# Kernel optimization log

Measured on AMD Instinct MI355X. Metric: run time of the kernel, lower is better.

Reference implementation:

```python
import jax, jax.numpy as jnp
import numpy as np
import math

B, L, D, H = 2, 2048, 1024, 16
HD = D // H          # head_dim = 64
DF = 4096            # d_feedforward
SIGMA = 0.02


def setup_inputs() -> dict:
    key = jax.random.key(0)
    ks = jax.random.split(key, 18)
    g = lambda k, shape: (jax.random.normal(k, shape, jnp.float32) * SIGMA)
    inp = {
        "x": jax.random.normal(ks[0], (B, L, D), jnp.float32),
        # causal mask: True above diagonal -> masked
        "causal_mask": jnp.triu(jnp.ones((L, L), dtype=bool), 1),
        # attention weights, stored [in, out] (math-equivalent to torch Linear)
        "Wq": g(ks[1], (D, D)), "bq": jnp.zeros((D,), jnp.float32),
        "Wk": g(ks[2], (D, D)), "bk": jnp.zeros((D,), jnp.float32),
        "Wv": g(ks[3], (D, D)), "bv": jnp.zeros((D,), jnp.float32),
        "Wo": g(ks[4], (D, D)), "bo": jnp.zeros((D,), jnp.float32),
        "ln1_g": jnp.ones((D,), jnp.float32), "ln1_b": jnp.zeros((D,), jnp.float32),
        "W1": g(ks[5], (D, DF)), "b1": jnp.zeros((DF,), jnp.float32),
        "W2": g(ks[6], (DF, D)), "b2": jnp.zeros((D,), jnp.float32),
        "ln2_g": jnp.ones((D,), jnp.float32), "ln2_b": jnp.zeros((D,), jnp.float32),
    }
    return inp


def _layernorm(x, g, b, eps=1e-5):
    m = jnp.mean(x, axis=-1, keepdims=True)
    v = jnp.mean((x - m) ** 2, axis=-1, keepdims=True)
    return (x - m) * jax.lax.rsqrt(v + eps) * g + b


def _rita_gelu(h):
    return h * 0.5 * (1.0 + jnp.tanh(0.79788456 * h * (1.0 + 0.044715 * h * h)))


def _rotate_half(x):
    x1, x2 = x[..., : x.shape[-1] // 2], x[..., x.shape[-1] // 2 :]
    return jnp.concatenate((-x2, x1), axis=-1)


def _rope_tables(seq_len, head_dim, dtype):
    inv_freq = 1.0 / (10000.0 ** (jnp.arange(0, head_dim, 2, dtype=jnp.float32) / head_dim))
    t = jnp.arange(seq_len, dtype=jnp.float32)
    freqs = jnp.einsum("i,j->ij", t, inv_freq)          # [L, HD/2]
    emb = jnp.concatenate((freqs, freqs), axis=-1)        # [L, HD]
    return jnp.cos(emb).astype(dtype)[None, None], jnp.sin(emb).astype(dtype)[None, None]


def reference(x, causal_mask, Wq, bq, Wk, bk, Wv, bv, Wo, bo,
              ln1_g, ln1_b, W1, b1, W2, b2, ln2_g, ln2_b):
    N, Lx, Dx = x.shape
    # --- attention block ---
    y = _layernorm(x, ln1_g, ln1_b)
    def heads(t):  # [N,L,D] -> [N,H,L,HD]
        return t.reshape(N, Lx, H, HD).transpose(0, 2, 1, 3)
    q = heads(y @ Wq + bq)
    k = heads(y @ Wk + bk)
    v = heads(y @ Wv + bv)
    cos, sin = _rope_tables(Lx, HD, x.dtype)
    q = q * cos + _rotate_half(q) * sin
    k = k * cos + _rotate_half(k) * sin
    att = jnp.einsum("nhqd,nhkd->nhqk", q, k) * (1.0 / math.sqrt(HD))
    att = jnp.where(causal_mask[None, None], jnp.float32(-jnp.inf).astype(att.dtype), att)
    att = jax.nn.softmax(att, axis=-1)
    o = jnp.einsum("nhqk,nhkd->nhqd", att, v)
    o = o.transpose(0, 2, 1, 3).reshape(N, Lx, Dx)
    y = o @ Wo + bo
    x = x + y
    # --- MLP block ---
    y = _layernorm(x, ln2_g, ln2_b)
    y = _rita_gelu(y @ W1 + b1) @ W2 + b2
    return x + y
```

## Files before the change

kernel.cpp:

```cpp
#include <hip/hip_runtime.h>
#include <math.h>

#define B_  2
#define L_  2048
#define D_  1024
#define H_  16
#define HD_ 64
#define DF_ 4096
#define NR_ 4096

typedef __bf16 bf16_t;
typedef bf16_t bf16x8 __attribute__((ext_vector_type(8)));
typedef float  f32x4  __attribute__((ext_vector_type(4)));
typedef unsigned short u16;
typedef u16 u16x8 __attribute__((ext_vector_type(8)));
typedef u16 u16x4 __attribute__((ext_vector_type(4)));

__device__ __forceinline__ u16 f2bf(float f) {
  unsigned u = __float_as_uint(f);
  u += 0x7fffu + ((u >> 16) & 1u);
  return (u16)(u >> 16);
}
__device__ __forceinline__ float bf2f(u16 s) {
  return __uint_as_float(((unsigned)s) << 16);
}
__device__ __forceinline__ float gelu_f(float h) {
  return h * 0.5f * (1.f + tanhf(0.79788456f * h * (1.f + 0.044715f * h * h)));
}

__device__ __forceinline__ void async_copy16(void* lds, const void* g) {
  __builtin_amdgcn_global_load_lds(
      (const __attribute__((address_space(1))) unsigned int*)g,
      (__attribute__((address_space(3))) unsigned int*)lds, 16, 0, 0);
}

__global__ __launch_bounds__(256) void transpose_conv(
    const float* __restrict__ W, u16* __restrict__ out, int K, int N) {
  __shared__ float T[64][65];
  const int tid = threadIdx.x;
  const int n0 = blockIdx.x * 64, k0 = blockIdx.y * 64;
  const int r = tid >> 2, c4 = (tid & 3) * 16;
  const float* src = W + (size_t)(k0 + r) * N + n0 + c4;
#pragma unroll
  for (int i = 0; i < 16; i += 4) {
    float4 f = *(const float4*)(src + i);
    T[r][c4 + i + 0] = f.x; T[r][c4 + i + 1] = f.y;
    T[r][c4 + i + 2] = f.z; T[r][c4 + i + 3] = f.w;
  }
  __syncthreads();
  u16* dst = out + (size_t)(n0 + r) * K + k0 + c4;
#pragma unroll
  for (int half = 0; half < 2; ++half) {
    u16x8 o8;
#pragma unroll
    for (int i = 0; i < 8; ++i) o8[i] = f2bf(T[c4 + half * 8 + i][r]);
    *(u16x8*)(dst + half * 8) = o8;
  }
}

__global__ __launch_bounds__(256) void concat_bias(
    const float* __restrict__ bq, const float* __restrict__ bk,
    const float* __restrict__ bv, float* __restrict__ bqkv) {
  int i = blockIdx.x * 256 + threadIdx.x;
  if (i < 3072) {
    float v = (i < 1024) ? bq[i] : (i < 2048) ? bk[i - 1024] : bv[i - 2048];
    bqkv[i] = v;
  }
}

__global__ __launch_bounds__(256) void rope_tables(
    float* __restrict__ cosT, float* __restrict__ sinT) {
  int i = blockIdx.x * 256 + threadIdx.x;
  int pos = i >> 5, d = i & 31;
  float invf = powf(10000.f, -(float)d / 32.f);
  float a = (float)pos * invf;
  cosT[i] = cosf(a);
  sinT[i] = sinf(a);
}

__global__ __launch_bounds__(256) void rope_apply(
    u16* __restrict__ qkv, const float* __restrict__ cosT,
    const float* __restrict__ sinT) {
  int i = blockIdx.x * 256 + threadIdx.x;
  int d0 = (i & 3) * 8;
  int hh = (i >> 2) & 15;
  int qk = (i >> 6) & 1;
  int row = i >> 7;
  int pos = row & (L_ - 1);
  size_t base = (size_t)row * 3072 + qk * 1024 + hh * 64 + d0;
  u16x8 a = *(const u16x8*)(qkv + base);
  u16x8 bb = *(const u16x8*)(qkv + base + 32);
  float4 c0 = *(const float4*)(cosT + pos * 32 + d0);
  float4 c1 = *(const float4*)(cosT + pos * 32 + d0 + 4);
  float4 s0 = *(const float4*)(sinT + pos * 32 + d0);
  float4 s1 = *(const float4*)(sinT + pos * 32 + d0 + 4);
  const float qs = qk ? 1.f : 0.125f;
  u16x8 ra, rb;
#pragma unroll
  for (int j = 0; j < 8; ++j) {
    float co = (j < 4) ? ((const float*)&c0)[j] : ((const float*)&c1)[j - 4];
    float si = (j < 4) ? ((const float*)&s0)[j] : ((const float*)&s1)[j - 4];
    float v0 = bf2f(a[j]), v1 = bf2f(bb[j]);
    ra[j] = f2bf((v0 * co - v1 * si) * qs);
    rb[j] = f2bf((v1 * co + v0 * si) * qs);
  }
  *(u16x8*)(qkv + base) = ra;
  *(u16x8*)(qkv + base + 32) = rb;
}

__global__ __launch_bounds__(256) void v_transpose(
    const u16* __restrict__ qkv, u16* __restrict__ vt) {
  const int tid = threadIdx.x;
  const int d = tid & 63, sub = tid >> 6;
  const int s0 = (blockIdx.x * 4 + sub) * 8;
  const int bh = blockIdx.y, b = bh >> 4, h = bh & 15;
  u16x8 o;
#pragma unroll
  for (int i = 0; i < 8; ++i)
    o[i] = qkv[(size_t)(b * L_ + s0 + i) * 3072 + 2048 + h * 64 + d];
  *(u16x8*)(vt + ((size_t)bh * 64 + d) * 2048 + s0) = o;
}

__global__ __launch_bounds__(256) void ln_kernel(
    const float* __restrict__ x, const float* __restrict__ gm,
    const float* __restrict__ bt, u16* __restrict__ out) {
  const int row = blockIdx.x, tid = threadIdx.x;
  const float4 v = ((const float4*)(x + (size_t)row * D_))[tid];
  float s = v.x + v.y + v.z + v.w;
#pragma unroll
  for (int m = 1; m < 64; m <<= 1) s += __shfl_xor(s, m);
  __shared__ float red[4], red2[4];
  if ((tid & 63) == 0) red[tid >> 6] = s;
  __syncthreads();
  const float mean = (red[0] + red[1] + red[2] + red[3]) * (1.f / D_);
  float d0 = v.x - mean, d1 = v.y - mean, d2 = v.z - mean, d3 = v.w - mean;
  float sq = d0 * d0 + d1 * d1 + d2 * d2 + d3 * d3;
#pragma unroll
  for (int m = 1; m < 64; m <<= 1) sq += __shfl_xor(sq, m);
  if ((tid & 63) == 0) red2[tid >> 6] = sq;
  __syncthreads();
  const float var = (red2[0] + red2[1] + red2[2] + red2[3]) * (1.f / D_);
  const float rstd = rsqrtf(var + 1e-5f);
  const int c = tid * 4;
  u16x4 o;
  o[0] = f2bf(d0 * rstd * gm[c + 0] + bt[c + 0]);
  o[1] = f2bf(d1 * rstd * gm[c + 1] + bt[c + 1]);
  o[2] = f2bf(d2 * rstd * gm[c + 2] + bt[c + 2]);
  o[3] = f2bf(d3 * rstd * gm[c + 3] + bt[c + 3]);
  ((u16x4*)(out + (size_t)row * D_))[tid] = o;
}

template <int EPI>
__global__ __launch_bounds__(256) void gemm_bt(
    const u16* __restrict__ A, const u16* __restrict__ Bt,
    const float* __restrict__ bias, const float* __restrict__ resid,
    void* __restrict__ out, int M, int N, int K) {
  __shared__ u16 As[128 * 32];
  __shared__ u16 Bs[128 * 32];
  const int tid = threadIdx.x;
  const int l = tid & 63, wid = tid >> 6;
  const int m0 = blockIdx.y * 128, n0 = blockIdx.x * 128;
  const int wr = wid >> 1, wc = wid & 1;

  f32x4 acc[4][4];
#pragma unroll
  for (int mi = 0; mi < 4; ++mi)
#pragma unroll
    for (int ni = 0; ni < 4; ++ni) acc[mi][ni] = (f32x4){0.f, 0.f, 0.f, 0.f};

  for (int kb = 0; kb < K; kb += 32) {
#pragma unroll
    for (int r = 0; r < 2; ++r) {
      const int fo = r * 4096 + tid * 16;
      const int row = fo >> 6, cb = fo & 63;
      async_copy16((char*)As + fo, A + (size_t)(m0 + row) * K + kb + (cb >> 1));
      async_copy16((char*)Bs + fo, Bt + (size_t)(n0 + row) * K + kb + (cb >> 1));
    }
    __syncthreads();
    bf16x8 ag[4], bg[4];
#pragma unroll
    for (int mi = 0; mi < 4; ++mi) {
      int row = wr * 64 + mi * 16 + (l & 15);
      ag[mi] = *(const bf16x8*)((const char*)As + row * 64 + ((l >> 4) * 16));
    }
#pragma unroll
    for (int ni = 0; ni < 4; ++ni) {
      int row = wc * 64 + ni * 16 + (l & 15);
      bg[ni] = *(const bf16x8*)((const char*)Bs + row * 64 + ((l >> 4) * 16));
    }
#pragma unroll
    for (int mi = 0; mi < 4; ++mi)
#pragma unroll
      for (int ni = 0; ni < 4; ++ni)
        acc[mi][ni] = __builtin_amdgcn_mfma_f32_16x16x32_bf16(
            ag[mi], bg[ni], acc[mi][ni], 0, 0, 0);
    __syncthreads();
  }

  const int cl = l & 15, rq = l >> 4;
#pragma unroll
  for (int ni = 0; ni < 4; ++ni) {
    const int col = n0 + wc * 64 + ni * 16 + cl;
    const float bv = bias[col];
#pragma unroll
    for (int mi = 0; mi < 4; ++mi) {
#pragma unroll
      for (int j = 0; j < 4; ++j) {
        const int rowg = m0 + wr * 64 + mi * 16 + rq * 4 + j;
        float v = acc[mi][ni][j] + bv;
        if (EPI == 0) {
          ((u16*)out)[(size_t)rowg * N + col] = f2bf(v);
        } else if (EPI == 1) {
          ((u16*)out)[(size_t)rowg * N + col] = f2bf(gelu_f(v));
        } else {
          ((float*)out)[(size_t)rowg * N + col] =
              v + resid[(size_t)rowg * N + col];
        }
      }
    }
  }
}

__global__ __launch_bounds__(256, 4) void attn_kernel(
    const u16* __restrict__ qkv, const u16* __restrict__ vt,
    u16* __restrict__ o) {
  const int tid = threadIdx.x, l = tid & 63, wid = tid >> 6;
  const int id = blockIdx.x;
  const int seq = id >> 3, xcd = id & 7;
  const int bh = xcd * 4 + (seq & 3);
  const int qblk = 31 - (seq >> 2);
  const int b = bh >> 4, h = bh & 15;
  const int q0 = qblk * 64;
  __shared__ u16 Ps[4][16 * 64];

  const int qrow_g = b * L_ + q0 + wid * 16 + (l & 15);
  const u16* qp = qkv + (size_t)qrow_g * 3072 + h * 64 + ((l >> 4) * 8);
  const bf16x8 qa0 = *(const bf16x8*)qp;
  const bf16x8 qa1 = *(const bf16x8*)(qp + 32);

  const u16* kbase = qkv + (size_t)(b * L_ + (l & 15)) * 3072 + 1024 + h * 64 +
                     ((l >> 4) * 8);
  const u16* vbase = vt + ((size_t)bh * 64 + (l & 15)) * 2048 + ((l >> 4) * 8);

  float m_[4], ls[4];
  f32x4 oa[4];
#pragma unroll
  for (int j = 0; j < 4; ++j) { m_[j] = -1e30f; ls[j] = 0.f; }
#pragma unroll
  for (int t = 0; t < 4; ++t) oa[t] = (f32x4){0.f, 0.f, 0.f, 0.f};

  char* const psw = (char*)&Ps[wid][0];
  const int rq4 = (l >> 4) << 2;

  for (int kb = 0; kb <= q0; kb += 64) {
    const bool diag = (kb == q0);

    bf16x8 kf[4][2];
#pragma unroll
    for (int t = 0; t < 4; ++t) {
      const u16* kp = kbase + (size_t)(kb + t * 16) * 3072;
      kf[t][0] = *(const bf16x8*)kp;
      kf[t][1] = *(const bf16x8*)(kp + 32);
    }

    float p[4][4];
#pragma unroll
    for (int t = 0; t < 4; ++t) {
      f32x4 s = (f32x4){0.f, 0.f, 0.f, 0.f};
      s = __builtin_amdgcn_mfma_f32_16x16x32_bf16(qa0, kf[t][0], s, 0, 0, 0);
      s = __builtin_amdgcn_mfma_f32_16x16x32_bf16(qa1, kf[t][1], s, 0, 0, 0);
      if (diag) {
        const int kcol = t * 16 + (l & 15);
        const int qrow = wid * 16 + rq4;
#pragma unroll
        for (int j = 0; j < 4; ++j)
          p[t][j] = (kcol <= qrow + j) ? s[j] : -1e30f;
      } else {
#pragma unroll
        for (int j = 0; j < 4; ++j) p[t][j] = s[j];
      }
    }

#pragma unroll
    for (int j = 0; j < 4; ++j) {
      float pm = fmaxf(fmaxf(p[0][j], p[1][j]), fmaxf(p[2][j], p[3][j]));
      pm = fmaxf(pm, __shfl_xor(pm, 1));
      pm = fmaxf(pm, __shfl_xor(pm, 2));
      pm = fmaxf(pm, __shfl_xor(pm, 4));
      pm = fmaxf(pm, __shfl_xor(pm, 8));
      const float mn = fmaxf(m_[j], pm);
      const float sc = __expf(m_[j] - mn);
      float rs = 0.f;
#pragma unroll
      for (int t = 0; t < 4; ++t) { p[t][j] = __expf(p[t][j] - mn); rs += p[t][j]; }
      rs += __shfl_xor(rs, 1);
      rs += __shfl_xor(rs, 2);
      rs += __shfl_xor(rs, 4);
      rs += __shfl_xor(rs, 8);
      ls[j] = ls[j] * sc + rs;
      m_[j] = mn;
#pragma unroll
      for (int t = 0; t < 4; ++t) oa[t][j] *= sc;
    }

#pragma unroll
    for (int t = 0; t < 4; ++t)
#pragma unroll
      for (int j = 0; j < 4; ++j) {
        const int rr = rq4 + j, cc = t * 16 + (l & 15);
        *(u16*)(psw + rr * 128 + ((cc * 2) ^ ((rr & 7) << 4))) = f2bf(p[t][j]);
      }

    bf16x8 vf[4][2];
#pragma unroll
    for (int t = 0; t < 4; ++t) {
      const u16* vp = vbase + (size_t)t * 16 * 2048 + kb;
      vf[t][0] = *(const bf16x8*)vp;
      vf[t][1] = *(const bf16x8*)(vp + 32);
    }

#pragma unroll
    for (int kc = 0; kc < 2; ++kc) {
      const int pr = l & 15, ke = kc * 32 + ((l >> 4) * 8);
      bf16x8 pf = *(const bf16x8*)(psw + pr * 128 + ((ke * 2) ^ ((pr & 7) << 4)));
#pragma unroll
      for (int t = 0; t < 4; ++t)
        oa[t] = __builtin_amdgcn_mfma_f32_16x16x32_bf16(pf, vf[t][kc], oa[t], 0, 0, 0);
    }
  }

#pragma unroll
  for (int j = 0; j < 4; ++j) {
    const float inv = 1.f / ls[j];
    const int rowg = b * L_ + q0 + wid * 16 + rq4 + j;
    u16* op = o + (size_t)rowg * D_ + h * 64 + (l & 15);
#pragma unroll
    for (int t = 0; t < 4; ++t) op[t * 16] = f2bf(oa[t][j] * inv);
  }
}

extern "C" void kernel_launch(void* const* d_in, const int* in_sizes, int n_in,
                              void* d_out, int out_size, void* d_ws, size_t ws_size,
                              hipStream_t stream) {
  (void)in_sizes; (void)n_in; (void)out_size; (void)ws_size;
  const float* x    = (const float*)d_in[0];
  const float* Wq   = (const float*)d_in[2];
  const float* bq   = (const float*)d_in[3];
  const float* Wk   = (const float*)d_in[4];
  const float* bk   = (const float*)d_in[5];
  const float* Wv   = (const float*)d_in[6];
  const float* bv   = (const float*)d_in[7];
  const float* Wo   = (const float*)d_in[8];
  const float* bo   = (const float*)d_in[9];
  const float* ln1g = (const float*)d_in[10];
  const float* ln1b = (const float*)d_in[11];
  const float* W1   = (const float*)d_in[12];
  const float* b1   = (const float*)d_in[13];
  const float* W2   = (const float*)d_in[14];
  const float* b2   = (const float*)d_in[15];
  const float* ln2g = (const float*)d_in[16];
  const float* ln2b = (const float*)d_in[17];
  float* out = (float*)d_out;
  char* ws = (char*)d_ws;

  u16*   wqkvT = (u16*)(ws + 0);
  u16*   woT   = (u16*)(ws + 6291456);
  u16*   w1T   = (u16*)(ws + 8388608);
  u16*   w2T   = (u16*)(ws + 16777216);
  float* bqkv  = (float*)(ws + 25165824);
  float* cosT  = (float*)(ws + 25178112);
  float* sinT  = (float*)(ws + 25440256);
  float* x2    = (float*)(ws + 25702400);
  u16*   lnbuf = (u16*)(ws + 42479616);
  u16*   vtb   = lnbuf;
  u16*   qkv   = (u16*)(ws + 50868224);
  u16*   attnO = (u16*)(ws + 76034048);
  u16*   hbuf  = qkv;

  const dim3 blk(256);
  transpose_conv<<<dim3(16, 16), blk, 0, stream>>>(Wq, wqkvT, 1024, 1024);
  transpose_conv<<<dim3(16, 16), blk, 0, stream>>>(Wk, wqkvT + 1024 * 1024, 1024, 1024);
  transpose_conv<<<dim3(16, 16), blk, 0, stream>>>(Wv, wqkvT + 2048 * 1024, 1024, 1024);
  transpose_conv<<<dim3(16, 16), blk, 0, stream>>>(Wo, woT, 1024, 1024);
  transpose_conv<<<dim3(64, 16), blk, 0, stream>>>(W1, w1T, 1024, 4096);
  transpose_conv<<<dim3(16, 64), blk, 0, stream>>>(W2, w2T, 4096, 1024);
  concat_bias<<<12, blk, 0, stream>>>(bq, bk, bv, bqkv);
  rope_tables<<<256, blk, 0, stream>>>(cosT, sinT);

  ln_kernel<<<NR_, blk, 0, stream>>>(x, ln1g, ln1b, lnbuf);
  gemm_bt<0><<<dim3(24, 32), blk, 0, stream>>>(lnbuf, wqkvT, bqkv, nullptr,
                                               qkv, NR_, 3072, 1024);
  rope_apply<<<2048, blk, 0, stream>>>(qkv, cosT, sinT);
  v_transpose<<<dim3(64, 32), blk, 0, stream>>>(qkv, vtb);
  attn_kernel<<<1024, blk, 0, stream>>>(qkv, vtb, attnO);

  gemm_bt<2><<<dim3(8, 32), blk, 0, stream>>>(attnO, woT, bo, x, x2,
                                              NR_, 1024, 1024);
  ln_kernel<<<NR_, blk, 0, stream>>>(x2, ln2g, ln2b, lnbuf);
  gemm_bt<1><<<dim3(32, 32), blk, 0, stream>>>(lnbuf, w1T, b1, nullptr,
                                               hbuf, NR_, 4096, 1024);
  gemm_bt<2><<<dim3(8, 32), blk, 0, stream>>>(hbuf, w2T, b2, x2, out,
                                              NR_, 1024, 4096);
}
```

Before: 549.8 us.

## Split-K atomic GEMMs for N=1024 projections and restructure attention softmax

The two N=1024 GEMMs (Wo and W2) become split-K launches with 2 and 4 K-slices. Their partial results are added with float atomics into an output that a new kernel pre-fills with residual plus bias. This targets low occupancy, since only 256 tiles cover the GPU. Attention is also rewritten to use transposed MFMA operands so each lane owns one query row, with the log2e scale folded into the Q scaling and exp2f used in softmax. This removes most cross-lane shuffles and skips fully masked diagonal tiles. The atomics make the results nondeterministic and add an extra elementwise pass over memory.

```diff
diff --git a/kernel.cpp b/kernel.cpp
--- a/kernel.cpp
+++ b/kernel.cpp
@@ -15,6 +15,8 @@
 typedef unsigned short u16;
 typedef u16 u16x8 __attribute__((ext_vector_type(8)));
 typedef u16 u16x4 __attribute__((ext_vector_type(4)));
+typedef unsigned int u32;
+typedef u32 u32x2 __attribute__((ext_vector_type(2)));
 
 __device__ __forceinline__ u16 f2bf(float f) {
   unsigned u = __float_as_uint(f);
@@ -94,7 +96,7 @@
   float4 c1 = *(const float4*)(cosT + pos * 32 + d0 + 4);
   float4 s0 = *(const float4*)(sinT + pos * 32 + d0);
   float4 s1 = *(const float4*)(sinT + pos * 32 + d0 + 4);
-  const float qs = qk ? 1.f : 0.125f;
+  const float qs = qk ? 1.f : 0.18033688f;
   u16x8 ra, rb;
 #pragma unroll
   for (int j = 0; j < 8; ++j) {
@@ -150,17 +152,30 @@
   ((u16x4*)(out + (size_t)row * D_))[tid] = o;
 }
 
+__global__ __launch_bounds__(256) void bias_resid_init(
+    const float* __restrict__ resid, const float* __restrict__ bias,
+    float* __restrict__ out) {
+  int i = blockIdx.x * 256 + threadIdx.x;
+  int c4 = (i & 255) * 4;
+  float4 r = ((const float4*)resid)[i];
+  float4 bv = *(const float4*)(bias + c4);
+  r.x += bv.x; r.y += bv.y; r.z += bv.z; r.w += bv.w;
+  ((float4*)out)[i] = r;
+}
+
 template <int EPI>
 __global__ __launch_bounds__(256) void gemm_bt(
     const u16* __restrict__ A, const u16* __restrict__ Bt,
-    const float* __restrict__ bias, const float* __restrict__ resid,
-    void* __restrict__ out, int M, int N, int K) {
+    const float* __restrict__ bias, void* __restrict__ out,
+    int M, int N, int K) {
   __shared__ u16 As[128 * 32];
   __shared__ u16 Bs[128 * 32];
   const int tid = threadIdx.x;
   const int l = tid & 63, wid = tid >> 6;
   const int m0 = blockIdx.y * 128, n0 = blockIdx.x * 128;
   const int wr = wid >> 1, wc = wid & 1;
+  const int ksub = K / gridDim.z;
+  const int k0 = blockIdx.z * ksub;
 
   f32x4 acc[4][4];
 #pragma unroll
@@ -168,7 +183,7 @@
 #pragma unroll
     for (int ni = 0; ni < 4; ++ni) acc[mi][ni] = (f32x4){0.f, 0.f, 0.f, 0.f};
 
-  for (int kb = 0; kb < K; kb += 32) {
+  for (int kb = k0; kb < k0 + ksub; kb += 32) {
 #pragma unroll
     for (int r = 0; r < 2; ++r) {
       const int fo = r * 4096 + tid * 16;
@@ -201,7 +216,7 @@
 #pragma unroll
   for (int ni = 0; ni < 4; ++ni) {
     const int col = n0 + wc * 64 + ni * 16 + cl;
-    const float bv = bias[col];
+    const float bv = (EPI == 3) ? 0.f : bias[col];
 #pragma unroll
     for (int mi = 0; mi < 4; ++mi) {
 #pragma unroll
@@ -213,8 +228,7 @@
         } else if (EPI == 1) {
           ((u16*)out)[(size_t)rowg * N + col] = f2bf(gelu_f(v));
         } else {
-          ((float*)out)[(size_t)rowg * N + col] =
-              v + resid[(size_t)rowg * N + col];
+          atomicAdd(&((float*)out)[(size_t)rowg * N + col], v);
         }
       }
     }
@@ -233,83 +247,48 @@
   const int q0 = qblk * 64;
   __shared__ u16 Ps[4][16 * 64];
 
-  const int qrow_g = b * L_ + q0 + wid * 16 + (l & 15);
-  const u16* qp = qkv + (size_t)qrow_g * 3072 + h * 64 + ((l >> 4) * 8);
-  const bf16x8 qa0 = *(const bf16x8*)qp;
-  const bf16x8 qa1 = *(const bf16x8*)(qp + 32);
-
-  const u16* kbase = qkv + (size_t)(b * L_ + (l & 15)) * 3072 + 1024 + h * 64 +
-                     ((l >> 4) * 8);
-  const u16* vbase = vt + ((size_t)bh * 64 + (l & 15)) * 2048 + ((l >> 4) * 8);
-
-  float m_[4], ls[4];
+  const int r16 = l & 15, g = l >> 4;
+
+  const int qrow_g = b * L_ + q0 + wid * 16 + r16;
+  const u16* qp = qkv + (size_t)qrow_g * 3072 + h * 64 + g * 8;
+  const bf16x8 qb0 = *(const bf16x8*)qp;
+  const bf16x8 qb1 = *(const bf16x8*)(qp + 32);
+
+  const u16* kbase = qkv + (size_t)(b * L_ + r16) * 3072 + 1024 + h * 64 + g * 8;
+  const u16* vbase = vt + ((size_t)bh * 64 + r16) * 2048 + g * 8;
+
+  float m_ = -1e30f, ls = 0.f;
   f32x4 oa[4];
 #pragma unroll
-  for (int j = 0; j < 4; ++j) { m_[j] = -1e30f; ls[j] = 0.f; }
-#pragma unroll
   for (int t = 0; t < 4; ++t) oa[t] = (f32x4){0.f, 0.f, 0.f, 0.f};
 
-  char* const psw = (char*)&Ps[wid][0];
-  const int rq4 = (l >> 4) << 2;
+  char* const psw = (char*)&Ps[wid][0] + r16 * 128;
+  const int pswz = (r16 & 7) << 4;
 
   for (int kb = 0; kb <= q0; kb += 64) {
     const bool diag = (kb == q0);
 
-    bf16x8 kf[4][2];
+    float p[4][4];
 #pragma unroll
     for (int t = 0; t < 4; ++t) {
+      if (diag && t > wid) {
+#pragma unroll
+        for (int j = 0; j < 4; ++j) p[t][j] = -1e30f;
+        continue;
+      }
       const u16* kp = kbase + (size_t)(kb + t * 16) * 3072;
-      kf[t][0] = *(const bf16x8*)kp;
-      kf[t][1] = *(const bf16x8*)(kp + 32);
-    }
-
-    float p[4][4];
-#pragma unroll
-    for (int t = 0; t < 4; ++t) {
       f32x4 s = (f32x4){0.f, 0.f, 0.f, 0.f};
-      s = __builtin_amdgcn_mfma_f32_16x16x32_bf16(qa0, kf[t][0], s, 0, 0, 0);
-      s = __builtin_amdgcn_mfma_f32_16x16x32_bf16(qa1, kf[t][1], s, 0, 0, 0);
-      if (diag) {
-        const int kcol = t * 16 + (l & 15);
-        const int qrow = wid * 16 + rq4;
+      s = __builtin_amdgcn_mfma_f32_16x16x32_bf16(*(const bf16x8*)kp, qb0, s, 0, 0, 0);
+      s = __builtin_amdgcn_mfma_f32_16x16x32_bf16(*(const bf16x8*)(kp + 32), qb1, s, 0, 0, 0);
+      if (diag && t == wid) {
 #pragma unroll
         for (int j = 0; j < 4; ++j)
-          p[t][j] = (kcol <= qrow + j) ? s[j] : -1e30f;
+          p[t][j] = (g * 4 + j <= r16) ? s[j] : -1e30f;
       } else {
 #pragma unroll
         for (int j = 0; j < 4; ++j) p[t][j] = s[j];
       }
     }
-
-#pragma unroll
-    for (int j = 0; j < 4; ++j) {
-      float pm = fmaxf(fmaxf(p[0][j], p[1][j]), fmaxf(p[2][j], p[3][j]));
-      pm = fmaxf(pm, __shfl_xor(pm, 1));
-      pm = fmaxf(pm, __shfl_xor(pm, 2));
-      pm = fmaxf(pm, __shfl_xor(pm, 4));
-      pm = fmaxf(pm, __shfl_xor(pm, 8));
-      const float mn = fmaxf(m_[j], pm);
-      const float sc = __expf(m_[j] - mn);
-      float rs = 0.f;
-#pragma unroll
-      for (int t = 0; t < 4; ++t) { p[t][j] = __expf(p[t][j] - mn); rs += p[t][j]; }
-      rs += __shfl_xor(rs, 1);
-      rs += __shfl_xor(rs, 2);
-      rs += __shfl_xor(rs, 4);
-      rs += __shfl_xor(rs, 8);
-      ls[j] = ls[j] * sc + rs;
-      m_[j] = mn;
-#pragma unroll
-      for (int t = 0; t < 4; ++t) oa[t][j] *= sc;
-    }
-
-#pragma unroll
-    for (int t = 0; t < 4; ++t)
-#pragma unroll
-      for (int j = 0; j < 4; ++j) {
-        const int rr = rq4 + j, cc = t * 16 + (l & 15);
-        *(u16*)(psw + rr * 128 + ((cc * 2) ^ ((rr & 7) << 4))) = f2bf(p[t][j]);
-      }
 
     bf16x8 vf[4][2];
 #pragma unroll
@@ -319,24 +298,51 @@
       vf[t][1] = *(const bf16x8*)(vp + 32);
     }
 
+    float pm = -1e30f;
+#pragma unroll
+    for (int t = 0; t < 4; ++t)
+#pragma unroll
+      for (int j = 0; j < 4; ++j) pm = fmaxf(pm, p[t][j]);
+    pm = fmaxf(pm, __shfl_xor(pm, 16));
+    pm = fmaxf(pm, __shfl_xor(pm, 32));
+    const float mn = fmaxf(m_, pm);
+    const float sc = exp2f(m_ - mn);
+    float rs = 0.f;
+#pragma unroll
+    for (int t = 0; t < 4; ++t)
+#pragma unroll
+      for (int j = 0; j < 4; ++j) { p[t][j] = exp2f(p[t][j] - mn); rs += p[t][j]; }
+    rs += __shfl_xor(rs, 16);
+    rs += __shfl_xor(rs, 32);
+    ls = ls * sc + rs;
+    m_ = mn;
+#pragma unroll
+    for (int t = 0; t < 4; ++t) oa[t] *= sc;
+
+#pragma unroll
+    for (int t = 0; t < 4; ++t) {
+      u32x2 w;
+      w[0] = (u32)f2bf(p[t][0]) | ((u32)f2bf(p[t][1]) << 16);
+      w[1] = (u32)f2bf(p[t][2]) | ((u32)f2bf(p[t][3]) << 16);
+      *(u32x2*)(psw + ((t * 32 + g * 8) ^ pswz)) = w;
+    }
+
 #pragma unroll
     for (int kc = 0; kc < 2; ++kc) {
-      const int pr = l & 15, ke = kc * 32 + ((l >> 4) * 8);
-      bf16x8 pf = *(const bf16x8*)(psw + pr * 128 + ((ke * 2) ^ ((pr & 7) << 4)));
+      bf16x8 pf = *(const bf16x8*)(psw + ((kc * 64 + g * 16) ^ pswz));
 #pragma unroll
       for (int t = 0; t < 4; ++t)
-        oa[t] = __builtin_amdgcn_mfma_f32_16x16x32_bf16(pf, vf[t][kc], oa[t], 0, 0, 0);
-    }
-  }
-
-#pragma unroll
-  for (int j = 0; j < 4; ++j) {
-    const float inv = 1.f / ls[j];
-    const int rowg = b * L_ + q0 + wid * 16 + rq4 + j;
-    u16* op = o + (size_t)rowg * D_ + h * 64 + (l & 15);
-#pragma unroll
-    for (int t = 0; t < 4; ++t) op[t * 16] = f2bf(oa[t][j] * inv);
-  }
+        oa[t] = __builtin_amdgcn_mfma_f32_16x16x32_bf16(vf[t][kc], pf, oa[t], 0, 0, 0);
+    }
+  }
+
+  const float inv = 1.f / ls;
+  u16* op = o + (size_t)qrow_g * D_ + h * 64;
+#pragma unroll
+  for (int t = 0; t < 4; ++t)
+#pragma unroll
+    for (int j = 0; j < 4; ++j)
+      op[t * 16 + g * 4 + j] = f2bf(oa[t][j] * inv);
 }
 
 extern "C" void kernel_launch(void* const* d_in, const int* in_sizes, int n_in,
@@ -388,17 +394,19 @@
   rope_tables<<<256, blk, 0, stream>>>(cosT, sinT);
 
   ln_kernel<<<NR_, blk, 0, stream>>>(x, ln1g, ln1b, lnbuf);
-  gemm_bt<0><<<dim3(24, 32), blk, 0, stream>>>(lnbuf, wqkvT, bqkv, nullptr,
-                                               qkv, NR_, 3072, 1024);
+  gemm_bt<0><<<dim3(24, 32, 1), blk, 0, stream>>>(lnbuf, wqkvT, bqkv,
+                                                  qkv, NR_, 3072, 1024);
   rope_apply<<<2048, blk, 0, stream>>>(qkv, cosT, sinT);
   v_transpose<<<dim3(64, 32), blk, 0, stream>>>(qkv, vtb);
   attn_kernel<<<1024, blk, 0, stream>>>(qkv, vtb, attnO);
 
-  gemm_bt<2><<<dim3(8, 32), blk, 0, stream>>>(attnO, woT, bo, x, x2,
-                                              NR_, 1024, 1024);
+  bias_resid_init<<<4096, blk, 0, stream>>>(x, bo, x2);
+  gemm_bt<3><<<dim3(8, 32, 2), blk, 0, stream>>>(attnO, woT, nullptr,
+                                                 x2, NR_, 1024, 1024);
   ln_kernel<<<NR_, blk, 0, stream>>>(x2, ln2g, ln2b, lnbuf);
-  gemm_bt<1><<<dim3(32, 32), blk, 0, stream>>>(lnbuf, w1T, b1, nullptr,
-                                               hbuf, NR_, 4096, 1024);
-  gemm_bt<2><<<dim3(8, 32), blk, 0, stream>>>(hbuf, w2T, b2, x2, out,
-                                              NR_, 1024, 4096);
-}
+  gemm_bt<1><<<dim3(32, 32, 1), blk, 0, stream>>>(lnbuf, w1T, b1,
+                                                  hbuf, NR_, 4096, 1024);
+  bias_resid_init<<<4096, blk, 0, stream>>>(x2, b2, out);
+  gemm_bt<3><<<dim3(8, 32, 4), blk, 0, stream>>>(hbuf, w2T, nullptr,
+                                                 out, NR_, 1024, 4096);
+}
```

Result: slower. 577.9 us (+5.1%).
